# Optimization experiments

Hardware: AMD Instinct MI355X
Metric: run time of the kernel (lower is better)

The kernel has to match this reference:

```python
import jax, jax.numpy as jnp
import numpy as np

N = 100000
E = 2000000
IN_DIM = 5
D = 32
L = 3
EPS = 1e-5


def setup_inputs() -> dict:
    key = jax.random.key(0)
    ks = jax.random.split(key, 10)
    x = jax.random.normal(ks[0], (N, IN_DIM), dtype=jnp.float32)
    edge_index = jax.random.randint(ks[1], (2, E), 0, N, dtype=jnp.int64)
    s = 1.0 / np.sqrt(D)
    w_in = jax.random.normal(ks[2], (D, IN_DIM), dtype=jnp.float32) / np.sqrt(IN_DIM)
    b_in = jnp.zeros((D,), dtype=jnp.float32)
    w_l = jax.random.normal(ks[3], (L, D, D), dtype=jnp.float32) * s  # lin_l per layer
    b_l = jnp.zeros((L, D), dtype=jnp.float32)
    w_r = jax.random.normal(ks[4], (L, D, D), dtype=jnp.float32) * s  # lin_r per layer (no bias, as in PyG SAGEConv)
    gamma = jnp.ones((D,), dtype=jnp.float32)
    beta = jnp.zeros((D,), dtype=jnp.float32)
    return {"x": x, "edge_index": edge_index, "w_in": w_in, "b_in": b_in,
            "w_l": w_l, "b_l": b_l, "w_r": w_r, "gamma": gamma, "beta": beta}


def _layernorm(h, gamma, beta):
    mu = jnp.mean(h, axis=-1, keepdims=True)
    var = jnp.mean(jnp.square(h - mu), axis=-1, keepdims=True)
    return (h - mu) * jax.lax.rsqrt(var + EPS) * gamma + beta


def reference(x, edge_index, w_in, b_in, w_l, b_l, w_r, gamma, beta):
    src = edge_index[0]
    dst = edge_index[1]
    n = x.shape[0]
    # node in-degree for mean aggregation (0-degree nodes get 0 output, like scatter_mean)
    deg = jax.ops.segment_sum(jnp.ones((src.shape[0],), dtype=x.dtype), dst, num_segments=n)
    inv_deg = (1.0 / jnp.maximum(deg, 1.0))[:, None]  # [N,1]
    h = x @ w_in.T + b_in  # [N, D]
    for i in range(w_l.shape[0]):
        msg = h[src]  # [E, D] gather
        agg = jax.ops.segment_sum(msg, dst, num_segments=n) * inv_deg  # mean aggregate
        h = agg @ w_l[i].T + b_l[i] + h @ w_r[i].T  # SAGEConv: lin_l(aggr) + lin_r(x)
        h = _layernorm(jax.nn.relu(h), gamma, beta)
    return h
```

## Files before the change

kernel.cpp:

```cpp
#include <hip/hip_runtime.h>
#include <hip/hip_bf16.h>

#define DIM 32
#define INDIM 5
#define EPB 4096
#define BKBITS 7
#define BKN 128
#define NBMAX 1024
#define CAP 4096

__device__ __forceinline__ unsigned short f2bf(float f) {
    unsigned u = __float_as_uint(f);
    u += 0x7FFFu + ((u >> 16) & 1u);
    return (unsigned short)(u >> 16);
}
__device__ __forceinline__ float bf2f_lo(unsigned u) { return __uint_as_float(u << 16); }
__device__ __forceinline__ float bf2f_hi(unsigned u) { return __uint_as_float(u & 0xFFFF0000u); }

__device__ __forceinline__ void acc_pk(float2& a01, float2& a23, float2& a45, float2& a67,
                                       uint4 v) {
    float2 v01, v23, v45, v67;
    v01.x = bf2f_lo(v.x); v01.y = bf2f_hi(v.x);
    v23.x = bf2f_lo(v.y); v23.y = bf2f_hi(v.y);
    v45.x = bf2f_lo(v.z); v45.y = bf2f_hi(v.z);
    v67.x = bf2f_lo(v.w); v67.y = bf2f_hi(v.w);
    asm volatile("v_pk_add_f32 %0, %0, %1" : "+v"(a01) : "v"(v01));
    asm volatile("v_pk_add_f32 %0, %0, %1" : "+v"(a23) : "v"(v23));
    asm volatile("v_pk_add_f32 %0, %0, %1" : "+v"(a45) : "v"(v45));
    asm volatile("v_pk_add_f32 %0, %0, %1" : "+v"(a67) : "v"(v67));
}


__global__ __launch_bounds__(256) void bucket_count_kernel(const int* __restrict__ dst,
                                                           int* __restrict__ bcnt, int e, int nb) {
    __shared__ int hist[NBMAX];
    int t = threadIdx.x;
    for (int i = t; i < nb; i += 256) hist[i] = 0;
    __syncthreads();
    int base = blockIdx.x * EPB;
    for (int k = 0; k < EPB; k += 256) {
        int i = base + k + t;
        if (i < e) {
            int dv = __builtin_nontemporal_load(&dst[i]);
            atomicAdd(&hist[dv >> BKBITS], 1);
        }
    }
    __syncthreads();
    for (int i = t; i < nb; i += 256) {
        int h = hist[i];
        if (h) atomicAdd(&bcnt[i], h);
    }
}


__global__ void bucket_scan_kernel(const int* __restrict__ bcnt, int* __restrict__ bbase,
                                   int* __restrict__ bcur, int* __restrict__ row_ptr,
                                   int nb, int n, int e) {
    __shared__ int s[1024];
    int t = threadIdx.x;
    int v = (t < nb) ? bcnt[t] : 0;
    s[t] = v;
    __syncthreads();
    for (int o = 1; o < 1024; o <<= 1) {
        int a = (t >= o) ? s[t - o] : 0;
        __syncthreads();
        s[t] += a;
        __syncthreads();
    }
    if (t < nb) {
        int excl = s[t] - v;
        bbase[t] = excl;
        bcur[t] = excl;
    }
    if (t == 0) {
        bbase[nb] = e;
        row_ptr[n] = e;
    }
}


__global__ __launch_bounds__(256) void bucket_fill_kernel(const int* __restrict__ src,
                                                          const int* __restrict__ dst,
                                                          int* __restrict__ bcur,
                                                          unsigned* __restrict__ packed,
                                                          int e, int nb) {
    __shared__ unsigned sw[EPB];
    __shared__ unsigned short sb[EPB];
    __shared__ int hist[NBMAX];
    __shared__ int rbase[NBMAX];
    int t = threadIdx.x;
    for (int i = t; i < nb; i += 256) hist[i] = 0;
    __syncthreads();
    int base = blockIdx.x * EPB;
    for (int k = 0; k < EPB; k += 256) {
        int i = base + k + t;
        if (i < e) {
            int s = __builtin_nontemporal_load(&src[i]);
            int d = __builtin_nontemporal_load(&dst[i]);
            int b = d >> BKBITS;
            sw[k + t] = ((unsigned)s << BKBITS) | (unsigned)(d & (BKN - 1));
            sb[k + t] = (unsigned short)b;
            atomicAdd(&hist[b], 1);
        }
    }
    __syncthreads();
    for (int i = t; i < nb; i += 256) {
        int h = hist[i];
        rbase[i] = h ? atomicAdd(&bcur[i], h) : 0;
        hist[i] = 0;
    }
    __syncthreads();
    for (int k = 0; k < EPB; k += 256) {
        int i = base + k + t;
        if (i < e) {
            int b = sb[k + t];
            int r = atomicAdd(&hist[b], 1);
            packed[rbase[b] + r] = sw[k + t];
        }
    }
}


__global__ __launch_bounds__(256) void csr_build_kernel(const unsigned* __restrict__ packed,
                                                        const int* __restrict__ bbase,
                                                        int* __restrict__ row_ptr,
                                                        int* __restrict__ esrc, int n) {
    __shared__ unsigned ew[CAP];
    __shared__ int h2[BKN];
    __shared__ int off[BKN];
    int b = blockIdx.x;
    int base = bbase[b];
    int cnt = bbase[b + 1] - base;
    int t = threadIdx.x;
    if (t < BKN) h2[t] = 0;
    __syncthreads();
    bool staged = (cnt <= CAP);
    for (int i = t; i < cnt; i += 256) {
        unsigned w = __builtin_nontemporal_load(&packed[base + i]);
        if (staged) ew[i] = w;
        atomicAdd(&h2[w & (BKN - 1)], 1);
    }
    __syncthreads();
    int v = 0;
    if (t < BKN) {
        v = h2[t];
        off[t] = v;
    }
    __syncthreads();
    for (int o = 1; o < BKN; o <<= 1) {
        int a = 0;
        if (t < BKN && t >= o) a = off[t - o];
        __syncthreads();
        if (t < BKN) off[t] += a;
        __syncthreads();
    }
    if (t < BKN) {
        int excl = off[t] - v;
        off[t] = excl;
        h2[t] = 0;
    }
    __syncthreads();
    int node = b * BKN + t;
    if (t < BKN && node < n) row_ptr[node] = base + off[t];
    for (int i = t; i < cnt; i += 256) {
        unsigned w = staged ? ew[i] : packed[base + i];
        int dl = w & (BKN - 1);
        int r = atomicAdd(&h2[dl], 1);
        esrc[base + off[dl] + r] = (int)(w >> BKBITS);
    }
}


__global__ void input_proj_kernel(const float* __restrict__ x, const float* __restrict__ w_in,
                                  const float* __restrict__ b_in,
                                  unsigned short* __restrict__ h, int n) {
    __shared__ float sw[DIM * INDIM];
    __shared__ float sb[DIM];
    int t = threadIdx.x;
    if (t < DIM * INDIM) sw[t] = w_in[t];
    if (t < DIM) sb[t] = b_in[t];
    __syncthreads();
    int idx = blockIdx.x * 256 + t;
    int node = idx >> 5;
    int d = idx & 31;
    if (node < n) {
        const float* xr = x + (size_t)node * INDIM;
        float acc = sb[d];
#pragma unroll
        for (int k = 0; k < INDIM; k++) acc = fmaf(xr[k], sw[d * INDIM + k], acc);
        h[(size_t)node * DIM + d] = f2bf(acc);
    }
}


template <int LAST>
__global__ __launch_bounds__(128, 3) void layer_fused_kernel(
    const int* __restrict__ row_ptr, const int* __restrict__ esrc,
    const unsigned short* __restrict__ h_in,
    unsigned short* __restrict__ h_out_bf, float* __restrict__ out_f32,
    const float* __restrict__ wl, const float* __restrict__ bl,
    const float* __restrict__ wr, const float* __restrict__ gamma,
    const float* __restrict__ beta, int n) {
    __shared__ float sAgg[32][DIM];
    __shared__ float sSelf[32][DIM];

    int t = threadIdx.x;
    int d = t & 31;

    int nd = t >> 2;
    int q = t & 3;
    int node = blockIdx.x * 32 + nd;
    const uint4* hv = (const uint4*)h_in;

    if (node < n) {
        {
            uint4 v = hv[(size_t)node * 4 + q];
            float4 f0 = make_float4(bf2f_lo(v.x), bf2f_hi(v.x), bf2f_lo(v.y), bf2f_hi(v.y));
            float4 f1 = make_float4(bf2f_lo(v.z), bf2f_hi(v.z), bf2f_lo(v.w), bf2f_hi(v.w));
            *(float4*)&sSelf[nd][q * 8] = f0;
            *(float4*)&sSelf[nd][q * 8 + 4] = f1;
        }
        int rs = row_ptr[node];
        int re = row_ptr[node + 1];
        float2 a01 = make_float2(0.f, 0.f), a23 = make_float2(0.f, 0.f);
        float2 a45 = make_float2(0.f, 0.f), a67 = make_float2(0.f, 0.f);
        int j = rs;
        int ids[16];
        bool have = (j + 16 <= re);
        if (have) {
#pragma unroll
            for (int k = 0; k < 16; k++) ids[k] = esrc[j + k];
        }
        while (have) {
            int jn = j + 16;
            bool haven = (jn + 16 <= re);
            uint4 vv[16];
#pragma unroll
            for (int k = 0; k < 16; k++) vv[k] = hv[(size_t)ids[k] * 4 + q];
            int nids[16];
            if (haven) {
#pragma unroll
                for (int k = 0; k < 16; k++) nids[k] = esrc[jn + k];
            }
#pragma unroll
            for (int k = 0; k < 16; k++) acc_pk(a01, a23, a45, a67, vv[k]);
            j = jn;
            have = haven;
            if (haven) {
#pragma unroll
                for (int k = 0; k < 16; k++) ids[k] = nids[k];
            }
        }
        if (j + 8 <= re) {
            int id8[8];
#pragma unroll
            for (int k = 0; k < 8; k++) id8[k] = esrc[j + k];
            uint4 vv[8];
#pragma unroll
            for (int k = 0; k < 8; k++) vv[k] = hv[(size_t)id8[k] * 4 + q];
#pragma unroll
            for (int k = 0; k < 8; k++) acc_pk(a01, a23, a45, a67, vv[k]);
            j += 8;
        }
        for (; j < re; ++j) {
            int s = esrc[j];
            uint4 v = hv[(size_t)s * 4 + q];
            acc_pk(a01, a23, a45, a67, v);
        }
        float iv = 1.f / fmaxf((float)(re - rs), 1.f);
        float4 f0 = make_float4(a01.x * iv, a01.y * iv, a23.x * iv, a23.y * iv);
        float4 f1 = make_float4(a45.x * iv, a45.y * iv, a67.x * iv, a67.y * iv);
        *(float4*)&sAgg[nd][q * 8] = f0;
        *(float4*)&sAgg[nd][q * 8 + 4] = f1;
    }
    __syncthreads();

    float wlr[DIM], wrr[DIM];
    {
        const float4* p1 = (const float4*)(wl + (size_t)d * DIM);
        const float4* p2 = (const float4*)(wr + (size_t)d * DIM);
#pragma unroll
        for (int qq = 0; qq < 8; qq++) {
            float4 a = p1[qq];
            wlr[4 * qq] = a.x; wlr[4 * qq + 1] = a.y; wlr[4 * qq + 2] = a.z; wlr[4 * qq + 3] = a.w;
            float4 c = p2[qq];
            wrr[4 * qq] = c.x; wrr[4 * qq + 1] = c.y; wrr[4 * qq + 2] = c.z; wrr[4 * qq + 3] = c.w;
        }
    }
    float bias = bl[d], g = gamma[d], be = beta[d];

#pragma unroll
    for (int it = 0; it < 8; ++it) {
        int ln = it * 4 + (t >> 5);
        int nodec = blockIdx.x * 32 + ln;
        if (nodec < n) {
            float o = bias;
            const float* va = sAgg[ln];
            const float* vs = sSelf[ln];
#pragma unroll
            for (int qq = 0; qq < 8; qq++) {
                float4 a = *(const float4*)&va[qq * 4];
                float4 s = *(const float4*)&vs[qq * 4];
                o = fmaf(a.x, wlr[4 * qq], o);     o = fmaf(s.x, wrr[4 * qq], o);
                o = fmaf(a.y, wlr[4 * qq + 1], o); o = fmaf(s.y, wrr[4 * qq + 1], o);
                o = fmaf(a.z, wlr[4 * qq + 2], o); o = fmaf(s.z, wrr[4 * qq + 2], o);
                o = fmaf(a.w, wlr[4 * qq + 3], o); o = fmaf(s.w, wrr[4 * qq + 3], o);
            }
            float out = fmaxf(o, 0.f);
            float sum = out, sq = out * out;
#pragma unroll
            for (int off = 16; off > 0; off >>= 1) {
                sum += __shfl_xor(sum, off, 32);
                sq += __shfl_xor(sq, off, 32);
            }
            float mu = sum * (1.f / 32.f);
            float var = fmaxf(sq * (1.f / 32.f) - mu * mu, 0.f);
            float r = rsqrtf(var + 1e-5f);
            float res = (out - mu) * r * g + be;
            if (LAST) out_f32[(size_t)nodec * DIM + d] = res;
            else      h_out_bf[(size_t)nodec * DIM + d] = f2bf(res);
        }
    }
}


extern "C" void kernel_launch(void* const* d_in, const int* in_sizes, int n_in,
                              void* d_out, int out_size, void* d_ws, size_t ws_size,
                              hipStream_t stream) {
    const float* x = (const float*)d_in[0];
    const int* ei = (const int*)d_in[1];
    const float* w_in = (const float*)d_in[2];
    const float* b_in = (const float*)d_in[3];
    const float* w_l = (const float*)d_in[4];
    const float* b_l = (const float*)d_in[5];
    const float* w_r = (const float*)d_in[6];
    const float* gamma = (const float*)d_in[7];
    const float* beta = (const float*)d_in[8];

    int n = in_sizes[0] / INDIM;
    int e = in_sizes[1] / 2;
    int L = in_sizes[4] / (DIM * DIM);
    const int* src = ei;
    const int* dst = ei + e;
    int nb = (n + BKN - 1) >> BKBITS;

    char* w = (char*)d_ws;
    int* bcnt = (int*)w;               w += (size_t)NBMAX * 4;
    int* bbase = (int*)w;              w += (size_t)(NBMAX + 1) * 4;
    int* bcur = (int*)w;               w += (size_t)NBMAX * 4;
    int* row_ptr = (int*)w;            w += (size_t)(n + 1) * 4;
    int* esrc = (int*)w;               w += (size_t)e * 4;
    unsigned short* h_A = (unsigned short*)w;  w += (size_t)n * DIM * 2;
    unsigned short* h_B = (unsigned short*)w;  w += (size_t)n * DIM * 2;
    unsigned* packed = (unsigned*)h_A;

    int nbE = (e + EPB - 1) / EPB;

    hipMemsetAsync(bcnt, 0, (size_t)nb * 4, stream);
    bucket_count_kernel<<<nbE, 256, 0, stream>>>(dst, bcnt, e, nb);
    bucket_scan_kernel<<<1, 1024, 0, stream>>>(bcnt, bbase, bcur, row_ptr, nb, n, e);
    bucket_fill_kernel<<<nbE, 256, 0, stream>>>(src, dst, bcur, packed, e, nb);
    csr_build_kernel<<<nb, 256, 0, stream>>>(packed, bbase, row_ptr, esrc, n);

    input_proj_kernel<<<(n * DIM + 255) / 256, 256, 0, stream>>>(x, w_in, b_in, h_A, n);

    unsigned short* bufs[2] = {h_A, h_B};
    int nbF = (n + 31) / 32;
    for (int i = 0; i < L; i++) {
        const unsigned short* hin = bufs[i & 1];
        unsigned short* hout = bufs[(i + 1) & 1];
        const float* wl = w_l + (size_t)i * DIM * DIM;
        const float* bl = b_l + (size_t)i * DIM;
        const float* wr = w_r + (size_t)i * DIM * DIM;
        if (i == L - 1)
            layer_fused_kernel<1><<<nbF, 128, 0, stream>>>(row_ptr, esrc, hin, nullptr,
                                                           (float*)d_out, wl, bl, wr,
                                                           gamma, beta, n);
        else
            layer_fused_kernel<0><<<nbF, 128, 0, stream>>>(row_ptr, esrc, hin, hout,
                                                           nullptr, wl, bl, wr,
                                                           gamma, beta, n);
    }
}
```

Baseline: 246.1 us.

## Sort nodes by degree to balance per-block work in fused SAGE layers

Adds a degree histogram, scan and scatter pass that builds a permutation of nodes grouped by in-degree. Each fused layer block then handles nodes of similar degree, which cuts wavefront divergence in the gather loop. The tail handling is also simplified into a single masked 16-wide batch, and the software prefetch of the next index batch is dropped. The cost is three extra small kernels, an indirection through perm, and less locality in row_ptr and esrc reads and output writes.

```diff
diff --git a/kernel.cpp b/kernel.cpp
--- a/kernel.cpp
+++ b/kernel.cpp
@@ -171,6 +171,50 @@
 }
 
 
+__global__ __launch_bounds__(256) void deg_hist_kernel(const int* __restrict__ row_ptr,
+                                                       int* __restrict__ dhist, int n) {
+    __shared__ int lh[256];
+    int t = threadIdx.x;
+    lh[t] = 0;
+    __syncthreads();
+    int idx = blockIdx.x * 256 + t;
+    if (idx < n) {
+        int dg = row_ptr[idx + 1] - row_ptr[idx];
+        if (dg > 255) dg = 255;
+        atomicAdd(&lh[dg], 1);
+    }
+    __syncthreads();
+    if (lh[t]) atomicAdd(&dhist[t], lh[t]);
+}
+
+__global__ void deg_scan_kernel(const int* __restrict__ dhist, int* __restrict__ dcur) {
+    __shared__ int s[256];
+    int t = threadIdx.x;
+    int v = dhist[t];
+    s[t] = v;
+    __syncthreads();
+    for (int o = 1; o < 256; o <<= 1) {
+        int a = (t >= o) ? s[t - o] : 0;
+        __syncthreads();
+        s[t] += a;
+        __syncthreads();
+    }
+    dcur[t] = s[t] - v;
+}
+
+__global__ __launch_bounds__(256) void perm_scatter_kernel(const int* __restrict__ row_ptr,
+                                                           int* __restrict__ dcur,
+                                                           int* __restrict__ perm, int n) {
+    int idx = blockIdx.x * 256 + threadIdx.x;
+    if (idx < n) {
+        int dg = row_ptr[idx + 1] - row_ptr[idx];
+        if (dg > 255) dg = 255;
+        int pos = atomicAdd(&dcur[dg], 1);
+        perm[pos] = idx;
+    }
+}
+
+
 __global__ void input_proj_kernel(const float* __restrict__ x, const float* __restrict__ w_in,
                                   const float* __restrict__ b_in,
                                   unsigned short* __restrict__ h, int n) {
@@ -196,6 +240,7 @@
 template <int LAST>
 __global__ __launch_bounds__(128, 3) void layer_fused_kernel(
     const int* __restrict__ row_ptr, const int* __restrict__ esrc,
+    const int* __restrict__ perm,
     const unsigned short* __restrict__ h_in,
     unsigned short* __restrict__ h_out_bf, float* __restrict__ out_f32,
     const float* __restrict__ wl, const float* __restrict__ bl,
@@ -203,16 +248,19 @@
     const float* __restrict__ beta, int n) {
     __shared__ float sAgg[32][DIM];
     __shared__ float sSelf[32][DIM];
+    __shared__ int sNode[32];
 
     int t = threadIdx.x;
     int d = t & 31;
 
     int nd = t >> 2;
     int q = t & 3;
-    int node = blockIdx.x * 32 + nd;
+    int slot = blockIdx.x * 32 + nd;
     const uint4* hv = (const uint4*)h_in;
 
-    if (node < n) {
+    if (slot < n) {
+        int node = perm[slot];
+        if (q == 0) sNode[nd] = node;
         {
             uint4 v = hv[(size_t)node * 4 + q];
             float4 f0 = make_float4(bf2f_lo(v.x), bf2f_hi(v.x), bf2f_lo(v.y), bf2f_hi(v.y));
@@ -225,47 +273,30 @@
         float2 a01 = make_float2(0.f, 0.f), a23 = make_float2(0.f, 0.f);
         float2 a45 = make_float2(0.f, 0.f), a67 = make_float2(0.f, 0.f);
         int j = rs;
-        int ids[16];
-        bool have = (j + 16 <= re);
-        if (have) {
+        for (; j + 16 <= re; j += 16) {
+            int ids[16];
 #pragma unroll
             for (int k = 0; k < 16; k++) ids[k] = esrc[j + k];
-        }
-        while (have) {
-            int jn = j + 16;
-            bool haven = (jn + 16 <= re);
             uint4 vv[16];
 #pragma unroll
             for (int k = 0; k < 16; k++) vv[k] = hv[(size_t)ids[k] * 4 + q];
-            int nids[16];
-            if (haven) {
-#pragma unroll
-                for (int k = 0; k < 16; k++) nids[k] = esrc[jn + k];
+#pragma unroll
+            for (int k = 0; k < 16; k++) acc_pk(a01, a23, a45, a67, vv[k]);
+        }
+        if (j < re) {
+            int m = re - j;
+            int ids[16];
+#pragma unroll
+            for (int k = 0; k < 16; k++) ids[k] = (k < m) ? esrc[j + k] : 0;
+            uint4 vv[16];
+#pragma unroll
+            for (int k = 0; k < 16; k++) vv[k] = hv[(size_t)ids[k] * 4 + q];
+#pragma unroll
+            for (int k = 0; k < 16; k++) {
+                uint4 v = vv[k];
+                if (k >= m) { v.x = 0u; v.y = 0u; v.z = 0u; v.w = 0u; }
+                acc_pk(a01, a23, a45, a67, v);
             }
-#pragma unroll
-            for (int k = 0; k < 16; k++) acc_pk(a01, a23, a45, a67, vv[k]);
-            j = jn;
-            have = haven;
-            if (haven) {
-#pragma unroll
-                for (int k = 0; k < 16; k++) ids[k] = nids[k];
-            }
-        }
-        if (j + 8 <= re) {
-            int id8[8];
-#pragma unroll
-            for (int k = 0; k < 8; k++) id8[k] = esrc[j + k];
-            uint4 vv[8];
-#pragma unroll
-            for (int k = 0; k < 8; k++) vv[k] = hv[(size_t)id8[k] * 4 + q];
-#pragma unroll
-            for (int k = 0; k < 8; k++) acc_pk(a01, a23, a45, a67, vv[k]);
-            j += 8;
-        }
-        for (; j < re; ++j) {
-            int s = esrc[j];
-            uint4 v = hv[(size_t)s * 4 + q];
-            acc_pk(a01, a23, a45, a67, v);
         }
         float iv = 1.f / fmaxf((float)(re - rs), 1.f);
         float4 f0 = make_float4(a01.x * iv, a01.y * iv, a23.x * iv, a23.y * iv);
@@ -292,8 +323,9 @@
 #pragma unroll
     for (int it = 0; it < 8; ++it) {
         int ln = it * 4 + (t >> 5);
-        int nodec = blockIdx.x * 32 + ln;
-        if (nodec < n) {
+        int slotc = blockIdx.x * 32 + ln;
+        if (slotc < n) {
+            int nodec = sNode[ln];
             float o = bias;
             const float* va = sAgg[ln];
             const float* vs = sSelf[ln];
@@ -346,21 +378,29 @@
 
     char* w = (char*)d_ws;
     int* bcnt = (int*)w;               w += (size_t)NBMAX * 4;
+    int* dhist = (int*)w;              w += 256 * 4;
+    int* dcur = (int*)w;               w += 256 * 4;
     int* bbase = (int*)w;              w += (size_t)(NBMAX + 1) * 4;
     int* bcur = (int*)w;               w += (size_t)NBMAX * 4;
     int* row_ptr = (int*)w;            w += (size_t)(n + 1) * 4;
     int* esrc = (int*)w;               w += (size_t)e * 4;
+    int* perm = (int*)w;               w += (size_t)n * 4;
     unsigned short* h_A = (unsigned short*)w;  w += (size_t)n * DIM * 2;
     unsigned short* h_B = (unsigned short*)w;  w += (size_t)n * DIM * 2;
     unsigned* packed = (unsigned*)h_A;
 
     int nbE = (e + EPB - 1) / EPB;
-
-    hipMemsetAsync(bcnt, 0, (size_t)nb * 4, stream);
+    int nbN = (n + 255) / 256;
+
+    hipMemsetAsync(bcnt, 0, (size_t)NBMAX * 4 + 256 * 4, stream);
     bucket_count_kernel<<<nbE, 256, 0, stream>>>(dst, bcnt, e, nb);
     bucket_scan_kernel<<<1, 1024, 0, stream>>>(bcnt, bbase, bcur, row_ptr, nb, n, e);
     bucket_fill_kernel<<<nbE, 256, 0, stream>>>(src, dst, bcur, packed, e, nb);
     csr_build_kernel<<<nb, 256, 0, stream>>>(packed, bbase, row_ptr, esrc, n);
+
+    deg_hist_kernel<<<nbN, 256, 0, stream>>>(row_ptr, dhist, n);
+    deg_scan_kernel<<<1, 256, 0, stream>>>(dhist, dcur);
+    perm_scatter_kernel<<<nbN, 256, 0, stream>>>(row_ptr, dcur, perm, n);
 
     input_proj_kernel<<<(n * DIM + 255) / 256, 256, 0, stream>>>(x, w_in, b_in, h_A, n);
 
@@ -373,11 +413,11 @@
         const float* bl = b_l + (size_t)i * DIM;
         const float* wr = w_r + (size_t)i * DIM * DIM;
         if (i == L - 1)
-            layer_fused_kernel<1><<<nbF, 128, 0, stream>>>(row_ptr, esrc, hin, nullptr,
+            layer_fused_kernel<1><<<nbF, 128, 0, stream>>>(row_ptr, esrc, perm, hin, nullptr,
                                                            (float*)d_out, wl, bl, wr,
                                                            gamma, beta, n);
         else
-            layer_fused_kernel<0><<<nbF, 128, 0, stream>>>(row_ptr, esrc, hin, hout,
+            layer_fused_kernel<0><<<nbF, 128, 0, stream>>>(row_ptr, esrc, perm, hin, hout,
                                                            nullptr, wl, bl, wr,
                                                            gamma, beta, n);
     }
```

After: 530.0 us. 2.15x slower.

## Shrink layer blocks to 16 nodes, simplify gather loop with masked tail, nontemporal IO

Applied to the files above, without the earlier changes.

The fused SAGE layer kernel now uses 64-thread blocks covering 16 nodes instead of 128 threads and 32 nodes, with launch bounds changed to allow more waves. The software-pipelined index prefetch is replaced by a plain 16-wide loop plus a single masked 16-wide tail that replaces the 8-wide and scalar remainders. Edge-index loads and output stores become nontemporal. The aim is lower register pressure, higher occupancy and fewer tail iterations. The cost is losing index prefetch overlap and issuing wasted gathers of node 0 in the tail.

```diff
diff --git a/kernel.cpp b/kernel.cpp
--- a/kernel.cpp
+++ b/kernel.cpp
@@ -194,22 +194,22 @@
 
 
 template <int LAST>
-__global__ __launch_bounds__(128, 3) void layer_fused_kernel(
+__global__ __launch_bounds__(64, 4) void layer_fused_kernel(
     const int* __restrict__ row_ptr, const int* __restrict__ esrc,
     const unsigned short* __restrict__ h_in,
     unsigned short* __restrict__ h_out_bf, float* __restrict__ out_f32,
     const float* __restrict__ wl, const float* __restrict__ bl,
     const float* __restrict__ wr, const float* __restrict__ gamma,
     const float* __restrict__ beta, int n) {
-    __shared__ float sAgg[32][DIM];
-    __shared__ float sSelf[32][DIM];
+    __shared__ float sAgg[16][DIM];
+    __shared__ float sSelf[16][DIM];
 
     int t = threadIdx.x;
     int d = t & 31;
 
     int nd = t >> 2;
     int q = t & 3;
-    int node = blockIdx.x * 32 + nd;
+    int node = blockIdx.x * 16 + nd;
     const uint4* hv = (const uint4*)h_in;
 
     if (node < n) {
@@ -225,47 +225,30 @@
         float2 a01 = make_float2(0.f, 0.f), a23 = make_float2(0.f, 0.f);
         float2 a45 = make_float2(0.f, 0.f), a67 = make_float2(0.f, 0.f);
         int j = rs;
-        int ids[16];
-        bool have = (j + 16 <= re);
-        if (have) {
-#pragma unroll
-            for (int k = 0; k < 16; k++) ids[k] = esrc[j + k];
-        }
-        while (have) {
-            int jn = j + 16;
-            bool haven = (jn + 16 <= re);
+        for (; j + 16 <= re; j += 16) {
+            int ids[16];
+#pragma unroll
+            for (int k = 0; k < 16; k++) ids[k] = __builtin_nontemporal_load(&esrc[j + k]);
             uint4 vv[16];
 #pragma unroll
             for (int k = 0; k < 16; k++) vv[k] = hv[(size_t)ids[k] * 4 + q];
-            int nids[16];
-            if (haven) {
-#pragma unroll
-                for (int k = 0; k < 16; k++) nids[k] = esrc[jn + k];
+#pragma unroll
+            for (int k = 0; k < 16; k++) acc_pk(a01, a23, a45, a67, vv[k]);
+        }
+        if (j < re) {
+            int m = re - j;
+            int ids[16];
+#pragma unroll
+            for (int k = 0; k < 16; k++) ids[k] = (k < m) ? __builtin_nontemporal_load(&esrc[j + k]) : 0;
+            uint4 vv[16];
+#pragma unroll
+            for (int k = 0; k < 16; k++) vv[k] = hv[(size_t)ids[k] * 4 + q];
+#pragma unroll
+            for (int k = 0; k < 16; k++) {
+                uint4 v = vv[k];
+                if (k >= m) { v.x = 0u; v.y = 0u; v.z = 0u; v.w = 0u; }
+                acc_pk(a01, a23, a45, a67, v);
             }
-#pragma unroll
-            for (int k = 0; k < 16; k++) acc_pk(a01, a23, a45, a67, vv[k]);
-            j = jn;
-            have = haven;
-            if (haven) {
-#pragma unroll
-                for (int k = 0; k < 16; k++) ids[k] = nids[k];
-            }
-        }
-        if (j + 8 <= re) {
-            int id8[8];
-#pragma unroll
-            for (int k = 0; k < 8; k++) id8[k] = esrc[j + k];
-            uint4 vv[8];
-#pragma unroll
-            for (int k = 0; k < 8; k++) vv[k] = hv[(size_t)id8[k] * 4 + q];
-#pragma unroll
-            for (int k = 0; k < 8; k++) acc_pk(a01, a23, a45, a67, vv[k]);
-            j += 8;
-        }
-        for (; j < re; ++j) {
-            int s = esrc[j];
-            uint4 v = hv[(size_t)s * 4 + q];
-            acc_pk(a01, a23, a45, a67, v);
         }
         float iv = 1.f / fmaxf((float)(re - rs), 1.f);
         float4 f0 = make_float4(a01.x * iv, a01.y * iv, a23.x * iv, a23.y * iv);
@@ -291,8 +274,8 @@
 
 #pragma unroll
     for (int it = 0; it < 8; ++it) {
-        int ln = it * 4 + (t >> 5);
-        int nodec = blockIdx.x * 32 + ln;
+        int ln = it * 2 + (t >> 5);
+        int nodec = blockIdx.x * 16 + ln;
         if (nodec < n) {
             float o = bias;
             const float* va = sAgg[ln];
@@ -317,8 +300,8 @@
             float var = fmaxf(sq * (1.f / 32.f) - mu * mu, 0.f);
             float r = rsqrtf(var + 1e-5f);
             float res = (out - mu) * r * g + be;
-            if (LAST) out_f32[(size_t)nodec * DIM + d] = res;
-            else      h_out_bf[(size_t)nodec * DIM + d] = f2bf(res);
+            if (LAST) __builtin_nontemporal_store(res, &out_f32[(size_t)nodec * DIM + d]);
+            else      __builtin_nontemporal_store(f2bf(res), &h_out_bf[(size_t)nodec * DIM + d]);
         }
     }
 }
@@ -365,7 +348,7 @@
     input_proj_kernel<<<(n * DIM + 255) / 256, 256, 0, stream>>>(x, w_in, b_in, h_A, n);
 
     unsigned short* bufs[2] = {h_A, h_B};
-    int nbF = (n + 31) / 32;
+    int nbF = (n + 15) / 16;
     for (int i = 0; i < L; i++) {
         const unsigned short* hin = bufs[i & 1];
         unsigned short* hout = bufs[(i + 1) & 1];
@@ -373,12 +356,12 @@
         const float* bl = b_l + (size_t)i * DIM;
         const float* wr = w_r + (size_t)i * DIM * DIM;
         if (i == L - 1)
-            layer_fused_kernel<1><<<nbF, 128, 0, stream>>>(row_ptr, esrc, hin, nullptr,
-                                                           (float*)d_out, wl, bl, wr,
-                                                           gamma, beta, n);
+            layer_fused_kernel<1><<<nbF, 64, 0, stream>>>(row_ptr, esrc, hin, nullptr,
+                                                          (float*)d_out, wl, bl, wr,
+                                                          gamma, beta, n);
         else
-            layer_fused_kernel<0><<<nbF, 128, 0, stream>>>(row_ptr, esrc, hin, hout,
-                                                           nullptr, wl, bl, wr,
-                                                           gamma, beta, n);
-    }
-}
+            layer_fused_kernel<0><<<nbF, 64, 0, stream>>>(row_ptr, esrc, hin, hout,
+                                                          nullptr, wl, bl, wr,
+                                                          gamma, beta, n);
+    }
+}
```

Measured after the change: 254.5 us. 1.03x slower.
